# Kernel tuning notes

Hardware: AMD Instinct MI355X
Metric: run time of the kernel (lower is better)

The kernel has to match this reference:

```python
import jax, jax.numpy as jnp
import numpy as np

N = 50000
E = 400000
IN = 128
OUT = 128
HID = 32
HEADS = 8
NEG_SLOPE = 0.2

_DIMS_IN = [IN, HID * HEADS, HID * HEADS, HID * HEADS]
_HEADS = [HEADS, HEADS, HEADS, 1]
_CH = [HID, HID, HID, OUT]


def setup_inputs() -> dict:
    key = jax.random.key(0)
    ks = list(jax.random.split(key, 32))
    kit = iter(ks)

    def p(shape, s=0.05):
        return (jax.random.normal(next(kit), shape, dtype=jnp.float32) * s)

    inp = {}
    inp["x"] = jax.random.normal(next(kit), (N, IN), dtype=jnp.float32)
    inp["edge_index"] = jax.random.randint(next(kit), (2, E), 0, N, dtype=jnp.int32)
    for i in range(4):
        hc = _HEADS[i] * _CH[i]
        inp[f"Wl{i}"] = p((hc, _DIMS_IN[i]))
        inp[f"bl{i}"] = p((hc,))
        inp[f"Wr{i}"] = p((hc, _DIMS_IN[i]))
        inp[f"br{i}"] = p((hc,))
        inp[f"att{i}"] = p((_HEADS[i], _CH[i]))
        inp[f"b{i}"] = p((hc,))
    return inp


def _gatv2_conv(x, src, dst, Wl, bl, Wr, br, att, bias, concat):
    # PyG GATv2Conv (share_weights=False, add_self_loops handled by caller).
    n = x.shape[0]
    H, C = att.shape
    xl = (x @ Wl.T + bl).reshape(n, H, C)  # source-side transform
    xr = (x @ Wr.T + br).reshape(n, H, C)  # dest-side transform
    e = jax.nn.leaky_relu(xl[src] + xr[dst], NEG_SLOPE)  # [E, H, C]
    logits = jnp.einsum('ehc,hc->eh', e, att)            # [E, H]
    # per-destination softmax (numerically stable via segment max)
    m = jax.ops.segment_max(logits, dst, num_segments=n)
    p = jnp.exp(logits - m[dst])
    denom = jax.ops.segment_sum(p, dst, num_segments=n)
    alpha = p / denom[dst]                                # [E, H]
    out = jax.ops.segment_sum(alpha[:, :, None] * xl[src], dst, num_segments=n)  # [N, H, C]
    out = out.reshape(n, H * C) if concat else out.mean(axis=1)
    return out + bias


def reference(x, edge_index, Wl0, bl0, Wr0, br0, att0, b0,
              Wl1, bl1, Wr1, br1, att1, b1,
              Wl2, bl2, Wr2, br2, att2, b2,
              Wl3, bl3, Wr3, br3, att3, b3):
    loop = jnp.arange(N, dtype=edge_index.dtype)  # default add_self_loops=True
    src = jnp.concatenate([edge_index[0], loop])
    dst = jnp.concatenate([edge_index[1], loop])
    layers = [
        (Wl0, bl0, Wr0, br0, att0, b0, True),
        (Wl1, bl1, Wr1, br1, att1, b1, True),
        (Wl2, bl2, Wr2, br2, att2, b2, True),
        (Wl3, bl3, Wr3, br3, att3, b3, False),
    ]
    h = x
    for params in layers[:-1]:
        res = h
        h = _gatv2_conv(h, src, dst, *params)
        h = jax.nn.elu(h)  # dropout is identity in eval mode
        if res.shape == h.shape:
            h = h + res
    return _gatv2_conv(h, src, dst, *layers[-1])
```

## Files before the change

kernel.cpp:

```cpp
#include <hip/hip_runtime.h>
#include <hip/hip_bf16.h>

constexpr int NN = 50000;
constexpr int NE = 400000;
constexpr int NE2 = NE + NN;
constexpr float NEG_SLOPE = 0.2f;
constexpr float LOG2E = 1.44269504f;

typedef __attribute__((ext_vector_type(8))) __bf16 bf16x8;
typedef __attribute__((ext_vector_type(4))) float f32x4;
typedef __attribute__((ext_vector_type(2))) float f32x2;

__device__ inline float bf2f(unsigned short u) { return __uint_as_float(((unsigned)u) << 16); }
__device__ inline unsigned short f2bf(float f) {
    unsigned x = __float_as_uint(f);
    return (unsigned short)((x + 0x7fffu + ((x >> 16) & 1u)) >> 16);
}
__device__ inline float bflo(unsigned u) { return __uint_as_float(u << 16); }
__device__ inline float bfhi(unsigned u) { return __uint_as_float(u & 0xffff0000u); }

__device__ inline void gload16(const unsigned short* g, unsigned short* l) {
    __builtin_amdgcn_global_load_lds(
        (const __attribute__((address_space(1))) unsigned int*)(g),
        (__attribute__((address_space(3))) unsigned int*)(l), 16, 0, 0);
}

__global__ void count_deg(const int* __restrict__ ei, int* __restrict__ deg) {
    int e = blockIdx.x * blockDim.x + threadIdx.x;
    if (e >= NE2) return;
    int dst = (e < NE) ? ei[NE + e] : (e - NE);
    atomicAdd(&deg[dst], 1);
}

constexpr int SCAN_NB = (NN + 1023) / 1024;

__global__ __launch_bounds__(1024) void scan_local(const int* __restrict__ deg,
                                                   int* __restrict__ row_ptr,
                                                   int* __restrict__ bsum) {
    __shared__ int wsum[16];
    const int t = threadIdx.x, lane = t & 63, w = t >> 6;
    const int i = blockIdx.x * 1024 + t;
    int v = (i < NN) ? deg[i] : 0;
    int x = v;
    #pragma unroll
    for (int off = 1; off < 64; off <<= 1) {
        int y = __shfl_up(x, off);
        if (lane >= off) x += y;
    }
    if (lane == 63) wsum[w] = x;
    __syncthreads();
    if (w == 0 && lane < 16) {
        int s = wsum[lane];
        #pragma unroll
        for (int off = 1; off < 16; off <<= 1) {
            int y = __shfl_up(s, off);
            if (lane >= off) s += y;
        }
        wsum[lane] = s;
    }
    __syncthreads();
    int excl = ((w == 0) ? 0 : wsum[w - 1]) + x - v;
    if (i < NN) row_ptr[i] = excl;
    if (t == 1023) bsum[blockIdx.x] = wsum[15];
}

__global__ void scan_bsums(int* __restrict__ bsum, int* __restrict__ row_ptr) {
    int lane = threadIdx.x;
    int v = (lane < SCAN_NB) ? bsum[lane] : 0;
    int x = v;
    #pragma unroll
    for (int off = 1; off < 64; off <<= 1) {
        int y = __shfl_up(x, off);
        if (lane >= off) x += y;
    }
    if (lane < SCAN_NB) bsum[lane] = x - v;
    if (lane == 63) row_ptr[NN] = x;
}

__global__ __launch_bounds__(1024) void scan_add(int* __restrict__ row_ptr,
                                                 int* __restrict__ cursor,
                                                 const int* __restrict__ bsum) {
    const int i = blockIdx.x * 1024 + threadIdx.x;
    if (i < NN) {
        int e = row_ptr[i] + bsum[blockIdx.x];
        row_ptr[i] = e;
        cursor[i] = e;
    }
}

__global__ void scatter_edges(const int* __restrict__ ei, int* __restrict__ cursor,
                              int* __restrict__ csr_src) {
    int e = blockIdx.x * blockDim.x + threadIdx.x;
    if (e >= NE2) return;
    int src, dst;
    if (e < NE) { src = ei[e]; dst = ei[NE + e]; }
    else        { src = dst = e - NE; }
    int pos = atomicAdd(&cursor[dst], 1);
    csr_src[pos] = src;
}

__global__ void f32_to_bf16(const float* __restrict__ in, unsigned short* __restrict__ out, int n4) {
    int i = blockIdx.x * blockDim.x + threadIdx.x;
    if (i >= n4) return;
    float4 v = *(const float4*)(in + 4 * (size_t)i);
    ushort4 o;
    o.x = f2bf(v.x); o.y = f2bf(v.y); o.z = f2bf(v.z); o.w = f2bf(v.w);
    *(ushort4*)(out + 4 * (size_t)i) = o;
}

__global__ void conv_weights(const float* __restrict__ w0l, const float* __restrict__ w0r,
                             const float* __restrict__ w1l, const float* __restrict__ w1r,
                             const float* __restrict__ w2l, const float* __restrict__ w2r,
                             const float* __restrict__ w3l, const float* __restrict__ w3r,
                             unsigned short* __restrict__ out) {
    int i = blockIdx.x * blockDim.x + threadIdx.x;
    const float* src; int base;
    if      (i < 8192)  { src = w0l; base = 0; }
    else if (i < 16384) { src = w0r; base = 8192; }
    else if (i < 32768) { src = w1l; base = 16384; }
    else if (i < 49152) { src = w1r; base = 32768; }
    else if (i < 65536) { src = w2l; base = 49152; }
    else if (i < 81920) { src = w2r; base = 65536; }
    else if (i < 90112) { src = w3l; base = 81920; }
    else                { src = w3r; base = 90112; }
    float4 v = ((const float4*)src)[i - base];
    ushort4 o;
    o.x = f2bf(v.x); o.y = f2bf(v.y); o.z = f2bf(v.z); o.w = f2bf(v.w);
    ((ushort4*)out)[i] = o;
}

#define GBM 128
#define GBN 128
#define GBK 64

__global__ __launch_bounds__(256) void gemm_fused(const unsigned short* __restrict__ A,
                                                  const unsigned short* __restrict__ Wc,
                                                  const float* __restrict__ bl,
                                                  const float* __restrict__ br,
                                                  unsigned short* __restrict__ outl,
                                                  unsigned short* __restrict__ outr,
                                                  int M, int Nhalf, int K, int lognx) {
    __shared__ __align__(16) unsigned short Alds[GBM * GBK];
    __shared__ __align__(16) unsigned short Wlds[GBN * GBK];
    const int nwg = gridDim.x;
    const int q = nwg >> 3, r8 = nwg & 7;
    const int xcd = blockIdx.x & 7, off = blockIdx.x >> 3;
    const int wg = (xcd < r8 ? xcd * (q + 1) : r8 * (q + 1) + (xcd - r8) * q) + off;
    const int nx = 1 << lognx;
    const int bm = (wg >> lognx) * GBM, bn = (wg & (nx - 1)) * GBN;

    const int tid = threadIdx.x;
    const int lane = tid & 63, wave = tid >> 6;
    const int wr = wave >> 1, wc = wave & 1;
    const int lrow = lane & 15, kgrp = lane >> 4;

    f32x4 acc[4][4] = {};

    for (int k0 = 0; k0 < K; k0 += GBK) {
        #pragma unroll
        for (int i = 0; i < 4; ++i) {
            int p = i * 256 + tid;
            int r = p >> 3, ck = p & 7;
            int sck = ck ^ (r & 7);
            int ga = bm + r; ga = (ga < M) ? ga : (M - 1);
            unsigned short* la = &Alds[(unsigned)(i * 256 + wave * 64) * 8];
            gload16(A + (size_t)ga * K + k0 + sck * 8, la);
            unsigned short* lw = &Wlds[(unsigned)(i * 256 + wave * 64) * 8];
            gload16(Wc + (size_t)(bn + r) * K + k0 + sck * 8, lw);
        }
        __syncthreads();
        #pragma unroll
        for (int kk = 0; kk < GBK; kk += 32) {
            bf16x8 av[4], bv[4];
            #pragma unroll
            for (int i = 0; i < 4; ++i) {
                int ar = wr * 64 + i * 16 + lrow;
                int ch = ((kk >> 3) + kgrp) ^ (ar & 7);
                av[i] = *(const bf16x8*)(&Alds[ar * GBK + ch * 8]);
            }
            #pragma unroll
            for (int j = 0; j < 4; ++j) {
                int brw = wc * 64 + j * 16 + lrow;
                int ch = ((kk >> 3) + kgrp) ^ (brw & 7);
                bv[j] = *(const bf16x8*)(&Wlds[brw * GBK + ch * 8]);
            }
            #pragma unroll
            for (int i = 0; i < 4; ++i)
                #pragma unroll
                for (int j = 0; j < 4; ++j)
                    acc[i][j] = __builtin_amdgcn_mfma_f32_16x16x32_bf16(bv[j], av[i], acc[i][j], 0, 0, 0);
        }
        __syncthreads();
    }

    const int half = (bn >= Nhalf) ? 1 : 0;
    unsigned short* outp = half ? outr : outl;
    const float* bp = half ? br : bl;
    const int cb = bn - half * Nhalf + wc * 64;
    #pragma unroll
    for (int i = 0; i < 4; ++i) {
        int row = bm + wr * 64 + i * 16 + lrow;
        if (row < M) {
            #pragma unroll
            for (int j = 0; j < 4; ++j) {
                int col = cb + j * 16 + kgrp * 4;
                float4 bb = *(const float4*)(bp + col);
                ushort4 o;
                o.x = f2bf(acc[i][j][0] + bb.x);
                o.y = f2bf(acc[i][j][1] + bb.y);
                o.z = f2bf(acc[i][j][2] + bb.z);
                o.w = f2bf(acc[i][j][3] + bb.w);
                *(ushort4*)(outp + (size_t)row * Nhalf + col) = o;
            }
        }
    }
}

template <int HC, int C, bool DO_ELU, bool DO_RES, bool OUT_F32>
__global__ __launch_bounds__(128) void gat_edge8(
        const unsigned short* __restrict__ xl,
        const unsigned short* __restrict__ xr,
        const float* __restrict__ att, const float* __restrict__ bias,
        const unsigned short* __restrict__ res, void* __restrict__ outp,
        const int* __restrict__ row_ptr, const int* __restrict__ csr_src) {
    constexpr int T = HC / 8;
    constexpr int NSL = 64 / T;
    constexpr int RW = C / 8;
    constexpr float THR = 11.54f;

    const int lane = threadIdx.x & 63;
    const int n = __builtin_amdgcn_readfirstlane((blockIdx.x << 1) | (threadIdx.x >> 6));
    const int w = lane / T;
    const int t = lane % T;
    const int ch = t * 8;
    const size_t base_r = (size_t)n * HC + ch;

    f32x2 xr2[4], av2[4], acc2[4];
    {
        uint4 u = *(const uint4*)(xr + base_r);
        xr2[0] = f32x2{bflo(u.x), bfhi(u.x)};
        xr2[1] = f32x2{bflo(u.y), bfhi(u.y)};
        xr2[2] = f32x2{bflo(u.z), bfhi(u.z)};
        xr2[3] = f32x2{bflo(u.w), bfhi(u.w)};
        float4 a0 = *(const float4*)(att + ch);
        float4 a1 = *(const float4*)(att + ch + 4);
        av2[0] = f32x2{a0.x, a0.y} * LOG2E;
        av2[1] = f32x2{a0.z, a0.w} * LOG2E;
        av2[2] = f32x2{a1.x, a1.y} * LOG2E;
        av2[3] = f32x2{a1.z, a1.w} * LOG2E;
        #pragma unroll
        for (int qi = 0; qi < 4; ++qi) acc2[qi] = f32x2{0.f, 0.f};
    }

    float m = -1e30f, d = 0.f;
    const int beg = row_ptr[n], end = row_ptr[n + 1];
    int e = beg + w;
    for (; e + NSL < end; e += 2 * NSL) {
        int s0 = csr_src[e], s1 = csr_src[e + NSL];
        uint4 g0 = *(const uint4*)(xl + (size_t)s0 * HC + ch);
        uint4 g1 = *(const uint4*)(xl + (size_t)s1 * HC + ch);
        f32x2 x0[4], x1[4];
        x0[0] = f32x2{bflo(g0.x), bfhi(g0.x)}; x0[1] = f32x2{bflo(g0.y), bfhi(g0.y)};
        x0[2] = f32x2{bflo(g0.z), bfhi(g0.z)}; x0[3] = f32x2{bflo(g0.w), bfhi(g0.w)};
        x1[0] = f32x2{bflo(g1.x), bfhi(g1.x)}; x1[1] = f32x2{bflo(g1.y), bfhi(g1.y)};
        x1[2] = f32x2{bflo(g1.z), bfhi(g1.z)}; x1[3] = f32x2{bflo(g1.w), bfhi(g1.w)};
        f32x2 p02 = {0.f, 0.f}, p12 = {0.f, 0.f};
        #pragma unroll
        for (int qi = 0; qi < 4; ++qi) {
            f32x2 u0 = x0[qi] + xr2[qi];
            f32x2 t0 = u0 * NEG_SLOPE;
            u0.x = fmaxf(u0.x, t0.x); u0.y = fmaxf(u0.y, t0.y);
            p02 = u0 * av2[qi] + p02;
            f32x2 u1 = x1[qi] + xr2[qi];
            f32x2 t1 = u1 * NEG_SLOPE;
            u1.x = fmaxf(u1.x, t1.x); u1.y = fmaxf(u1.y, t1.y);
            p12 = u1 * av2[qi] + p12;
        }
        float p0 = p02.x + p02.y, p1 = p12.x + p12.y;
        #pragma unroll
        for (int mm = RW / 2; mm >= 1; mm >>= 1) {
            p0 += __shfl_xor(p0, mm);
            p1 += __shfl_xor(p1, mm);
        }
        float pmax = fmaxf(p0, p1);
        if (__any(pmax > m + THR)) {
            float mn = fmaxf(m, pmax);
            float sc = exp2f(m - mn);
            float e0 = exp2f(p0 - mn), e1 = exp2f(p1 - mn);
            d = d * sc + e0 + e1;
            f32x2 sc2 = {sc, sc}, e02 = {e0, e0}, e12 = {e1, e1};
            #pragma unroll
            for (int qi = 0; qi < 4; ++qi)
                acc2[qi] = acc2[qi] * sc2 + (x0[qi] * e02 + x1[qi] * e12);
            m = mn;
        } else {
            float e0 = exp2f(p0 - m), e1 = exp2f(p1 - m);
            d += e0 + e1;
            f32x2 e02 = {e0, e0}, e12 = {e1, e1};
            #pragma unroll
            for (int qi = 0; qi < 4; ++qi)
                acc2[qi] = acc2[qi] + (x0[qi] * e02 + x1[qi] * e12);
        }
    }
    if (e < end) {
        int s0 = csr_src[e];
        uint4 g0 = *(const uint4*)(xl + (size_t)s0 * HC + ch);
        f32x2 x0[4];
        x0[0] = f32x2{bflo(g0.x), bfhi(g0.x)}; x0[1] = f32x2{bflo(g0.y), bfhi(g0.y)};
        x0[2] = f32x2{bflo(g0.z), bfhi(g0.z)}; x0[3] = f32x2{bflo(g0.w), bfhi(g0.w)};
        f32x2 p02 = {0.f, 0.f};
        #pragma unroll
        for (int qi = 0; qi < 4; ++qi) {
            f32x2 u0 = x0[qi] + xr2[qi];
            f32x2 t0 = u0 * NEG_SLOPE;
            u0.x = fmaxf(u0.x, t0.x); u0.y = fmaxf(u0.y, t0.y);
            p02 = u0 * av2[qi] + p02;
        }
        float p0 = p02.x + p02.y;
        #pragma unroll
        for (int mm = RW / 2; mm >= 1; mm >>= 1) p0 += __shfl_xor(p0, mm);
        if (__any(p0 > m + THR)) {
            float mn = fmaxf(m, p0);
            float sc = exp2f(m - mn);
            float e0 = exp2f(p0 - mn);
            d = d * sc + e0;
            f32x2 sc2 = {sc, sc}, e02 = {e0, e0};
            #pragma unroll
            for (int qi = 0; qi < 4; ++qi) acc2[qi] = acc2[qi] * sc2 + x0[qi] * e02;
            m = mn;
        } else {
            float e0 = exp2f(p0 - m);
            d += e0;
            f32x2 e02 = {e0, e0};
            #pragma unroll
            for (int qi = 0; qi < 4; ++qi) acc2[qi] = acc2[qi] + x0[qi] * e02;
        }
    }

    #pragma unroll
    for (int st = T; st < 64; st <<= 1) {
        float mo = __shfl_xor(m, st);
        float do_ = __shfl_xor(d, st);
        float ao[8];
        #pragma unroll
        for (int qi = 0; qi < 4; ++qi) {
            ao[2 * qi]     = __shfl_xor(acc2[qi].x, st);
            ao[2 * qi + 1] = __shfl_xor(acc2[qi].y, st);
        }
        float mn = fmaxf(m, mo);
        float s0 = exp2f(m - mn), s1 = exp2f(mo - mn);
        d = d * s0 + do_ * s1;
        #pragma unroll
        for (int qi = 0; qi < 4; ++qi) {
            acc2[qi].x = acc2[qi].x * s0 + ao[2 * qi] * s1;
            acc2[qi].y = acc2[qi].y * s0 + ao[2 * qi + 1] * s1;
        }
        m = mn;
    }

    if (lane < T) {
        float inv = 1.f / d;
        float o[8];
        float4 b0 = *(const float4*)(bias + ch);
        float4 b1 = *(const float4*)(bias + ch + 4);
        o[0] = acc2[0].x * inv + b0.x; o[1] = acc2[0].y * inv + b0.y;
        o[2] = acc2[1].x * inv + b0.z; o[3] = acc2[1].y * inv + b0.w;
        o[4] = acc2[2].x * inv + b1.x; o[5] = acc2[2].y * inv + b1.y;
        o[6] = acc2[3].x * inv + b1.z; o[7] = acc2[3].y * inv + b1.w;
        if constexpr (DO_ELU) {
            #pragma unroll
            for (int v = 0; v < 8; ++v)
                o[v] = o[v] > 0.f ? o[v] : exp2f(o[v] * LOG2E) - 1.f;
        }
        if constexpr (DO_RES) {
            uint4 ru = *(const uint4*)(res + base_r);
            o[0] += bflo(ru.x); o[1] += bfhi(ru.x);
            o[2] += bflo(ru.y); o[3] += bfhi(ru.y);
            o[4] += bflo(ru.z); o[5] += bfhi(ru.z);
            o[6] += bflo(ru.w); o[7] += bfhi(ru.w);
        }
        if constexpr (OUT_F32) {
            float* op = (float*)outp + base_r;
            *(float4*)(op)     = make_float4(o[0], o[1], o[2], o[3]);
            *(float4*)(op + 4) = make_float4(o[4], o[5], o[6], o[7]);
        } else {
            uint4 u;
            u.x = (unsigned)f2bf(o[0]) | ((unsigned)f2bf(o[1]) << 16);
            u.y = (unsigned)f2bf(o[2]) | ((unsigned)f2bf(o[3]) << 16);
            u.z = (unsigned)f2bf(o[4]) | ((unsigned)f2bf(o[5]) << 16);
            u.w = (unsigned)f2bf(o[6]) | ((unsigned)f2bf(o[7]) << 16);
            *(uint4*)((unsigned short*)outp + base_r) = u;
        }
    }
}

extern "C" void kernel_launch(void* const* d_in, const int* in_sizes, int n_in,
                              void* d_out, int out_size, void* d_ws, size_t ws_size,
                              hipStream_t stream) {
    const float* x  = (const float*)d_in[0];
    const int*   ei = (const int*)d_in[1];
    auto P = [&](int layer, int j) { return (const float*)d_in[2 + 6 * layer + j]; };

    unsigned short* x_bf = (unsigned short*)d_ws;
    unsigned short* h0 = x_bf + (size_t)NN * 128;
    unsigned short* h1 = h0 + (size_t)NN * 256;
    unsigned short* xl = h1 + (size_t)NN * 256;
    unsigned short* xr = xl + (size_t)NN * 256;
    unsigned short* Wb = xr + (size_t)NN * 256;
    int* csr_src = (int*)(Wb + 393216);
    int* row_ptr = csr_src + NE2;
    int* cursor  = row_ptr + (NN + 1);
    int* deg     = cursor + NN;
    int* bsum    = deg + NN;

    hipMemsetAsync(deg, 0, NN * sizeof(int), stream);
    int eb = (NE2 + 255) / 256;
    count_deg<<<eb, 256, 0, stream>>>(ei, deg);
    scan_local<<<SCAN_NB, 1024, 0, stream>>>(deg, row_ptr, bsum);
    scan_bsums<<<1, 64, 0, stream>>>(bsum, row_ptr);
    scan_add<<<SCAN_NB, 1024, 0, stream>>>(row_ptr, cursor, bsum);
    scatter_edges<<<eb, 256, 0, stream>>>(ei, cursor, csr_src);

    conv_weights<<<384, 256, 0, stream>>>(P(0, 0), P(0, 2), P(1, 0), P(1, 2),
                                          P(2, 0), P(2, 2), P(3, 0), P(3, 2), Wb);
    int n4 = NN * 128 / 4;
    f32_to_bf16<<<(n4 + 255) / 256, 256, 0, stream>>>(x, x_bf, n4);

    const int mb = (NN + GBM - 1) / GBM;
    const int nwgL = 4 * mb, nwgLast = 2 * mb;
    const int gat_g = NN / 2;

    gemm_fused<<<nwgL, 256, 0, stream>>>(x_bf, Wb + 0,      P(0, 1), P(0, 3), xl, xr, NN, 256, 128, 2);
    gat_edge8<256, 32, true, false, false><<<gat_g, 128, 0, stream>>>(xl, xr, P(0, 4), P(0, 5),
                                                                      nullptr, h0, row_ptr, csr_src);
    gemm_fused<<<nwgL, 256, 0, stream>>>(h0,   Wb + 65536,  P(1, 1), P(1, 3), xl, xr, NN, 256, 256, 2);
    gat_edge8<256, 32, true, true, false><<<gat_g, 128, 0, stream>>>(xl, xr, P(1, 4), P(1, 5),
                                                                     h0, h1, row_ptr, csr_src);
    gemm_fused<<<nwgL, 256, 0, stream>>>(h1,   Wb + 196608, P(2, 1), P(2, 3), xl, xr, NN, 256, 256, 2);
    gat_edge8<256, 32, true, true, false><<<gat_g, 128, 0, stream>>>(xl, xr, P(2, 4), P(2, 5),
                                                                     h1, h0, row_ptr, csr_src);
    gemm_fused<<<nwgLast, 256, 0, stream>>>(h0, Wb + 327680, P(3, 1), P(3, 3), xl, xr, NN, 128, 256, 1);
    gat_edge8<128, 128, false, false, true><<<gat_g, 128, 0, stream>>>(xl, xr, P(3, 4), P(3, 5),
                                                                       nullptr, d_out, row_ptr, csr_src);
}
```

Measured before the change: 395.4 us.

## Restructure GAT edge kernel to one node per block with 4-channel lanes

Replaces the two-nodes-per-block edge aggregation kernel, where each lane handled 8 channels, with a one-node-per-block kernel where each thread handles 4 channels and 2 or 4 edge slices run across waves. The main loop now processes four edges per iteration to raise memory-level parallelism, and partial online-softmax states are merged through shared memory instead of cross-lane shuffles. This adds a __syncthreads and shared-memory traffic per node, uses narrower 8-byte gathers, and doubles the block count. With only about nine edges per node, many slices may sit idle.

```diff
diff --git a/kernel.cpp b/kernel.cpp
--- a/kernel.cpp
+++ b/kernel.cpp
@@ -9,15 +9,12 @@
 
 typedef __attribute__((ext_vector_type(8))) __bf16 bf16x8;
 typedef __attribute__((ext_vector_type(4))) float f32x4;
-typedef __attribute__((ext_vector_type(2))) float f32x2;
 
 __device__ inline float bf2f(unsigned short u) { return __uint_as_float(((unsigned)u) << 16); }
 __device__ inline unsigned short f2bf(float f) {
     unsigned x = __float_as_uint(f);
     return (unsigned short)((x + 0x7fffu + ((x >> 16) & 1u)) >> 16);
 }
-__device__ inline float bflo(unsigned u) { return __uint_as_float(u << 16); }
-__device__ inline float bfhi(unsigned u) { return __uint_as_float(u & 0xffff0000u); }
 
 __device__ inline void gload16(const unsigned short* g, unsigned short* l) {
     __builtin_amdgcn_global_load_lds(
@@ -216,67 +213,101 @@
     }
 }
 
-template <int HC, int C, bool DO_ELU, bool DO_RES, bool OUT_F32>
-__global__ __launch_bounds__(128) void gat_edge8(
+template <int H, int C, int NW, bool DO_ELU, bool DO_RES, bool OUT_F32>
+__global__ __launch_bounds__(128) void gat_edge4(
         const unsigned short* __restrict__ xl,
         const unsigned short* __restrict__ xr,
         const float* __restrict__ att, const float* __restrict__ bias,
         const unsigned short* __restrict__ res, void* __restrict__ outp,
         const int* __restrict__ row_ptr, const int* __restrict__ csr_src) {
-    constexpr int T = HC / 8;
-    constexpr int NSL = 64 / T;
-    constexpr int RW = C / 8;
+    constexpr int HC = H * C;
+    constexpr int T = HC / 4;
+    constexpr int RW = C / 4;
     constexpr float THR = 11.54f;
-
-    const int lane = threadIdx.x & 63;
-    const int n = __builtin_amdgcn_readfirstlane((blockIdx.x << 1) | (threadIdx.x >> 6));
-    const int w = lane / T;
-    const int t = lane % T;
-    const int ch = t * 8;
+    __shared__ float smem[NW * T * 6];
+
+    const int n = blockIdx.x;
+    const int tid = threadIdx.x;
+    const int w = tid / T;
+    const int t = tid % T;
+    const int ch = 4 * t;
     const size_t base_r = (size_t)n * HC + ch;
 
-    f32x2 xr2[4], av2[4], acc2[4];
+    float xr4[4], av[4], acc[4] = {0.f, 0.f, 0.f, 0.f};
     {
-        uint4 u = *(const uint4*)(xr + base_r);
-        xr2[0] = f32x2{bflo(u.x), bfhi(u.x)};
-        xr2[1] = f32x2{bflo(u.y), bfhi(u.y)};
-        xr2[2] = f32x2{bflo(u.z), bfhi(u.z)};
-        xr2[3] = f32x2{bflo(u.w), bfhi(u.w)};
-        float4 a0 = *(const float4*)(att + ch);
-        float4 a1 = *(const float4*)(att + ch + 4);
-        av2[0] = f32x2{a0.x, a0.y} * LOG2E;
-        av2[1] = f32x2{a0.z, a0.w} * LOG2E;
-        av2[2] = f32x2{a1.x, a1.y} * LOG2E;
-        av2[3] = f32x2{a1.z, a1.w} * LOG2E;
-        #pragma unroll
-        for (int qi = 0; qi < 4; ++qi) acc2[qi] = f32x2{0.f, 0.f};
+        ushort4 u = *(const ushort4*)(xr + base_r);
+        xr4[0] = bf2f(u.x); xr4[1] = bf2f(u.y); xr4[2] = bf2f(u.z); xr4[3] = bf2f(u.w);
+        float4 a = *(const float4*)(att + ch);
+        av[0] = a.x * LOG2E; av[1] = a.y * LOG2E; av[2] = a.z * LOG2E; av[3] = a.w * LOG2E;
     }
 
     float m = -1e30f, d = 0.f;
     const int beg = row_ptr[n], end = row_ptr[n + 1];
-    int e = beg + w;
-    for (; e + NSL < end; e += 2 * NSL) {
-        int s0 = csr_src[e], s1 = csr_src[e + NSL];
-        uint4 g0 = *(const uint4*)(xl + (size_t)s0 * HC + ch);
-        uint4 g1 = *(const uint4*)(xl + (size_t)s1 * HC + ch);
-        f32x2 x0[4], x1[4];
-        x0[0] = f32x2{bflo(g0.x), bfhi(g0.x)}; x0[1] = f32x2{bflo(g0.y), bfhi(g0.y)};
-        x0[2] = f32x2{bflo(g0.z), bfhi(g0.z)}; x0[3] = f32x2{bflo(g0.w), bfhi(g0.w)};
-        x1[0] = f32x2{bflo(g1.x), bfhi(g1.x)}; x1[1] = f32x2{bflo(g1.y), bfhi(g1.y)};
-        x1[2] = f32x2{bflo(g1.z), bfhi(g1.z)}; x1[3] = f32x2{bflo(g1.w), bfhi(g1.w)};
-        f32x2 p02 = {0.f, 0.f}, p12 = {0.f, 0.f};
-        #pragma unroll
-        for (int qi = 0; qi < 4; ++qi) {
-            f32x2 u0 = x0[qi] + xr2[qi];
-            f32x2 t0 = u0 * NEG_SLOPE;
-            u0.x = fmaxf(u0.x, t0.x); u0.y = fmaxf(u0.y, t0.y);
-            p02 = u0 * av2[qi] + p02;
-            f32x2 u1 = x1[qi] + xr2[qi];
-            f32x2 t1 = u1 * NEG_SLOPE;
-            u1.x = fmaxf(u1.x, t1.x); u1.y = fmaxf(u1.y, t1.y);
-            p12 = u1 * av2[qi] + p12;
-        }
-        float p0 = p02.x + p02.y, p1 = p12.x + p12.y;
+    const int nmain = (end - beg) / (4 * NW);
+
+    for (int g = 0; g < nmain; ++g) {
+        const int base = beg + (g * NW + w) * 4;
+        int s[4];
+        #pragma unroll
+        for (int k = 0; k < 4; ++k) s[k] = csr_src[base + k];
+        ushort4 gx[4];
+        #pragma unroll
+        for (int k = 0; k < 4; ++k) gx[k] = *(const ushort4*)(xl + (size_t)s[k] * HC + ch);
+        float xv[4][4], p[4];
+        #pragma unroll
+        for (int k = 0; k < 4; ++k) {
+            xv[k][0] = bf2f(gx[k].x); xv[k][1] = bf2f(gx[k].y);
+            xv[k][2] = bf2f(gx[k].z); xv[k][3] = bf2f(gx[k].w);
+            float pp = 0.f;
+            #pragma unroll
+            for (int q = 0; q < 4; ++q) {
+                float u = xv[k][q] + xr4[q];
+                u = fmaxf(u, u * NEG_SLOPE);
+                pp = fmaf(u, av[q], pp);
+            }
+            p[k] = pp;
+        }
+        #pragma unroll
+        for (int mm = RW / 2; mm >= 1; mm >>= 1) {
+            #pragma unroll
+            for (int k = 0; k < 4; ++k) p[k] += __shfl_xor(p[k], mm);
+        }
+        float pmax = fmaxf(fmaxf(p[0], p[1]), fmaxf(p[2], p[3]));
+        if (__any(pmax > m + THR)) {
+            float mn = fmaxf(m, pmax);
+            float sc = exp2f(m - mn);
+            float e0 = exp2f(p[0] - mn), e1 = exp2f(p[1] - mn);
+            float e2 = exp2f(p[2] - mn), e3 = exp2f(p[3] - mn);
+            d = d * sc + (e0 + e1) + (e2 + e3);
+            #pragma unroll
+            for (int q = 0; q < 4; ++q)
+                acc[q] = acc[q] * sc + (xv[0][q] * e0 + xv[1][q] * e1)
+                                     + (xv[2][q] * e2 + xv[3][q] * e3);
+            m = mn;
+        } else {
+            float e0 = exp2f(p[0] - m), e1 = exp2f(p[1] - m);
+            float e2 = exp2f(p[2] - m), e3 = exp2f(p[3] - m);
+            d += (e0 + e1) + (e2 + e3);
+            #pragma unroll
+            for (int q = 0; q < 4; ++q)
+                acc[q] += (xv[0][q] * e0 + xv[1][q] * e1) + (xv[2][q] * e2 + xv[3][q] * e3);
+        }
+    }
+
+    int e = beg + nmain * 4 * NW + w;
+    for (; e + NW < end; e += 2 * NW) {
+        int s0 = csr_src[e], s1 = csr_src[e + NW];
+        ushort4 g0 = *(const ushort4*)(xl + (size_t)s0 * HC + ch);
+        ushort4 g1 = *(const ushort4*)(xl + (size_t)s1 * HC + ch);
+        float x0[4], x1[4];
+        x0[0] = bf2f(g0.x); x0[1] = bf2f(g0.y); x0[2] = bf2f(g0.z); x0[3] = bf2f(g0.w);
+        x1[0] = bf2f(g1.x); x1[1] = bf2f(g1.y); x1[2] = bf2f(g1.z); x1[3] = bf2f(g1.w);
+        float p0 = 0.f, p1 = 0.f;
+        #pragma unroll
+        for (int q = 0; q < 4; ++q) {
+            float u0 = x0[q] + xr4[q]; u0 = fmaxf(u0, u0 * NEG_SLOPE); p0 = fmaf(u0, av[q], p0);
+            float u1 = x1[q] + xr4[q]; u1 = fmaxf(u1, u1 * NEG_SLOPE); p1 = fmaf(u1, av[q], p1);
+        }
         #pragma unroll
         for (int mm = RW / 2; mm >= 1; mm >>= 1) {
             p0 += __shfl_xor(p0, mm);
@@ -288,35 +319,26 @@
             float sc = exp2f(m - mn);
             float e0 = exp2f(p0 - mn), e1 = exp2f(p1 - mn);
             d = d * sc + e0 + e1;
-            f32x2 sc2 = {sc, sc}, e02 = {e0, e0}, e12 = {e1, e1};
-            #pragma unroll
-            for (int qi = 0; qi < 4; ++qi)
-                acc2[qi] = acc2[qi] * sc2 + (x0[qi] * e02 + x1[qi] * e12);
+            #pragma unroll
+            for (int q = 0; q < 4; ++q) acc[q] = acc[q] * sc + x0[q] * e0 + x1[q] * e1;
             m = mn;
         } else {
             float e0 = exp2f(p0 - m), e1 = exp2f(p1 - m);
             d += e0 + e1;
-            f32x2 e02 = {e0, e0}, e12 = {e1, e1};
-            #pragma unroll
-            for (int qi = 0; qi < 4; ++qi)
-                acc2[qi] = acc2[qi] + (x0[qi] * e02 + x1[qi] * e12);
+            #pragma unroll
+            for (int q = 0; q < 4; ++q) acc[q] += x0[q] * e0 + x1[q] * e1;
         }
     }
     if (e < end) {
         int s0 = csr_src[e];
-        uint4 g0 = *(const uint4*)(xl + (size_t)s0 * HC + ch);
-        f32x2 x0[4];
-        x0[0] = f32x2{bflo(g0.x), bfhi(g0.x)}; x0[1] = f32x2{bflo(g0.y), bfhi(g0.y)};
-        x0[2] = f32x2{bflo(g0.z), bfhi(g0.z)}; x0[3] = f32x2{bflo(g0.w), bfhi(g0.w)};
-        f32x2 p02 = {0.f, 0.f};
-        #pragma unroll
-        for (int qi = 0; qi < 4; ++qi) {
-            f32x2 u0 = x0[qi] + xr2[qi];
-            f32x2 t0 = u0 * NEG_SLOPE;
-            u0.x = fmaxf(u0.x, t0.x); u0.y = fmaxf(u0.y, t0.y);
-            p02 = u0 * av2[qi] + p02;
-        }
-        float p0 = p02.x + p02.y;
+        ushort4 g0 = *(const ushort4*)(xl + (size_t)s0 * HC + ch);
+        float x0[4];
+        x0[0] = bf2f(g0.x); x0[1] = bf2f(g0.y); x0[2] = bf2f(g0.z); x0[3] = bf2f(g0.w);
+        float p0 = 0.f;
+        #pragma unroll
+        for (int q = 0; q < 4; ++q) {
+            float u0 = x0[q] + xr4[q]; u0 = fmaxf(u0, u0 * NEG_SLOPE); p0 = fmaf(u0, av[q], p0);
+        }
         #pragma unroll
         for (int mm = RW / 2; mm >= 1; mm >>= 1) p0 += __shfl_xor(p0, mm);
         if (__any(p0 > m + THR)) {
@@ -324,72 +346,53 @@
             float sc = exp2f(m - mn);
             float e0 = exp2f(p0 - mn);
             d = d * sc + e0;
-            f32x2 sc2 = {sc, sc}, e02 = {e0, e0};
-            #pragma unroll
-            for (int qi = 0; qi < 4; ++qi) acc2[qi] = acc2[qi] * sc2 + x0[qi] * e02;
+            #pragma unroll
+            for (int q = 0; q < 4; ++q) acc[q] = acc[q] * sc + x0[q] * e0;
             m = mn;
         } else {
             float e0 = exp2f(p0 - m);
             d += e0;
-            f32x2 e02 = {e0, e0};
-            #pragma unroll
-            for (int qi = 0; qi < 4; ++qi) acc2[qi] = acc2[qi] + x0[qi] * e02;
-        }
-    }
-
-    #pragma unroll
-    for (int st = T; st < 64; st <<= 1) {
-        float mo = __shfl_xor(m, st);
-        float do_ = __shfl_xor(d, st);
-        float ao[8];
-        #pragma unroll
-        for (int qi = 0; qi < 4; ++qi) {
-            ao[2 * qi]     = __shfl_xor(acc2[qi].x, st);
-            ao[2 * qi + 1] = __shfl_xor(acc2[qi].y, st);
-        }
-        float mn = fmaxf(m, mo);
-        float s0 = exp2f(m - mn), s1 = exp2f(mo - mn);
-        d = d * s0 + do_ * s1;
-        #pragma unroll
-        for (int qi = 0; qi < 4; ++qi) {
-            acc2[qi].x = acc2[qi].x * s0 + ao[2 * qi] * s1;
-            acc2[qi].y = acc2[qi].y * s0 + ao[2 * qi + 1] * s1;
-        }
-        m = mn;
-    }
-
-    if (lane < T) {
+            #pragma unroll
+            for (int q = 0; q < 4; ++q) acc[q] += x0[q] * e0;
+        }
+    }
+
+    float* st = &smem[(w * T + t) * 6];
+    st[0] = m; st[1] = d;
+    st[2] = acc[0]; st[3] = acc[1]; st[4] = acc[2]; st[5] = acc[3];
+    __syncthreads();
+    if (w == 0) {
+        #pragma unroll
+        for (int o = 1; o < NW; ++o) {
+            const float* so = &smem[(o * T + t) * 6];
+            float mo = so[0], dd = so[1];
+            float mn = fmaxf(m, mo);
+            float s0 = exp2f(m - mn), s1 = exp2f(mo - mn);
+            d = d * s0 + dd * s1;
+            #pragma unroll
+            for (int q = 0; q < 4; ++q) acc[q] = acc[q] * s0 + so[2 + q] * s1;
+            m = mn;
+        }
         float inv = 1.f / d;
-        float o[8];
-        float4 b0 = *(const float4*)(bias + ch);
-        float4 b1 = *(const float4*)(bias + ch + 4);
-        o[0] = acc2[0].x * inv + b0.x; o[1] = acc2[0].y * inv + b0.y;
-        o[2] = acc2[1].x * inv + b0.z; o[3] = acc2[1].y * inv + b0.w;
-        o[4] = acc2[2].x * inv + b1.x; o[5] = acc2[2].y * inv + b1.y;
-        o[6] = acc2[3].x * inv + b1.z; o[7] = acc2[3].y * inv + b1.w;
+        float4 b = *(const float4*)(bias + ch);
+        float o0 = acc[0] * inv + b.x, o1 = acc[1] * inv + b.y;
+        float o2 = acc[2] * inv + b.z, o3 = acc[3] * inv + b.w;
         if constexpr (DO_ELU) {
-            #pragma unroll
-            for (int v = 0; v < 8; ++v)
-                o[v] = o[v] > 0.f ? o[v] : exp2f(o[v] * LOG2E) - 1.f;
+            o0 = o0 > 0.f ? o0 : exp2f(o0 * LOG2E) - 1.f;
+            o1 = o1 > 0.f ? o1 : exp2f(o1 * LOG2E) - 1.f;
+            o2 = o2 > 0.f ? o2 : exp2f(o2 * LOG2E) - 1.f;
+            o3 = o3 > 0.f ? o3 : exp2f(o3 * LOG2E) - 1.f;
         }
         if constexpr (DO_RES) {
-            uint4 ru = *(const uint4*)(res + base_r);
-            o[0] += bflo(ru.x); o[1] += bfhi(ru.x);
-            o[2] += bflo(ru.y); o[3] += bfhi(ru.y);
-            o[4] += bflo(ru.z); o[5] += bfhi(ru.z);
-            o[6] += bflo(ru.w); o[7] += bfhi(ru.w);
+            ushort4 ru = *(const ushort4*)(res + base_r);
+            o0 += bf2f(ru.x); o1 += bf2f(ru.y); o2 += bf2f(ru.z); o3 += bf2f(ru.w);
         }
         if constexpr (OUT_F32) {
-            float* op = (float*)outp + base_r;
-            *(float4*)(op)     = make_float4(o[0], o[1], o[2], o[3]);
-            *(float4*)(op + 4) = make_float4(o[4], o[5], o[6], o[7]);
+            *(float4*)((float*)outp + base_r) = make_float4(o0, o1, o2, o3);
         } else {
-            uint4 u;
-            u.x = (unsigned)f2bf(o[0]) | ((unsigned)f2bf(o[1]) << 16);
-            u.y = (unsigned)f2bf(o[2]) | ((unsigned)f2bf(o[3]) << 16);
-            u.z = (unsigned)f2bf(o[4]) | ((unsigned)f2bf(o[5]) << 16);
-            u.w = (unsigned)f2bf(o[6]) | ((unsigned)f2bf(o[7]) << 16);
-            *(uint4*)((unsigned short*)outp + base_r) = u;
+            ushort4 u;
+            u.x = f2bf(o0); u.y = f2bf(o1); u.z = f2bf(o2); u.w = f2bf(o3);
+            *(ushort4*)((unsigned short*)outp + base_r) = u;
         }
     }
 }
@@ -428,18 +431,17 @@
 
     const int mb = (NN + GBM - 1) / GBM;
     const int nwgL = 4 * mb, nwgLast = 2 * mb;
-    const int gat_g = NN / 2;
 
     gemm_fused<<<nwgL, 256, 0, stream>>>(x_bf, Wb + 0,      P(0, 1), P(0, 3), xl, xr, NN, 256, 128, 2);
-    gat_edge8<256, 32, true, false, false><<<gat_g, 128, 0, stream>>>(xl, xr, P(0, 4), P(0, 5),
-                                                                      nullptr, h0, row_ptr, csr_src);
+    gat_edge4<8, 32, 2, true, false, false><<<NN, 128, 0, stream>>>(xl, xr, P(0, 4), P(0, 5),
+                                                                    nullptr, h0, row_ptr, csr_src);
     gemm_fused<<<nwgL, 256, 0, stream>>>(h0,   Wb + 65536,  P(1, 1), P(1, 3), xl, xr, NN, 256, 256, 2);
-    gat_edge8<256, 32, true, true, false><<<gat_g, 128, 0, stream>>>(xl, xr, P(1, 4), P(1, 5),
-                                                                     h0, h1, row_ptr, csr_src);
+    gat_edge4<8, 32, 2, true, true, false><<<NN, 128, 0, stream>>>(xl, xr, P(1, 4), P(1, 5),
+                                                                   h0, h1, row_ptr, csr_src);
     gemm_fused<<<nwgL, 256, 0, stream>>>(h1,   Wb + 196608, P(2, 1), P(2, 3), xl, xr, NN, 256, 256, 2);
-    gat_edge8<256, 32, true, true, false><<<gat_g, 128, 0, stream>>>(xl, xr, P(2, 4), P(2, 5),
-                                                                     h1, h0, row_ptr, csr_src);
+    gat_edge4<8, 32, 2, true, true, false><<<NN, 128, 0, stream>>>(xl, xr, P(2, 4), P(2, 5),
+                                                                   h1, h0, row_ptr, csr_src);
     gemm_fused<<<nwgLast, 256, 0, stream>>>(h0, Wb + 327680, P(3, 1), P(3, 3), xl, xr, NN, 128, 256, 1);
-    gat_edge8<128, 128, false, false, true><<<gat_g, 128, 0, stream>>>(xl, xr, P(3, 4), P(3, 5),
-                                                                       nullptr, d_out, row_ptr, csr_src);
-}
+    gat_edge4<1, 128, 4, false, false, true><<<NN, 128, 0, stream>>>(xl, xr, P(3, 4), P(3, 5),
+                                                                     nullptr, d_out, row_ptr, csr_src);
+}
```

New measurement: 420.1 us. 6.2% more time.
